# Kernel tuning notes

Measured on AMD Instinct MI355X. Metric: run time of the kernel, lower is better.

## Reference

```python
import jax, jax.numpy as jnp
import numpy as np

DIM = 1024
DIM_HEAD = 64
HEADS = 16
NUM_LATENTS = 64
INNER = DIM_HEAD * HEADS  # 1024


def setup_inputs() -> dict:
    key = jax.random.key(0)
    ks = jax.random.split(key, 6)
    b, m, n = 8, 4, 1024
    x = jax.random.normal(ks[0], (b, m, n, DIM), dtype=jnp.float32)
    latents = jax.random.normal(ks[1], (NUM_LATENTS, DIM), dtype=jnp.float32)
    # Linear weights stored as (in, out); no bias for q/kv, bias for out (matches nn.Linear defaults)
    Wq = jax.random.normal(ks[2], (DIM, INNER), dtype=jnp.float32) * (DIM ** -0.5)
    Wkv = jax.random.normal(ks[3], (DIM, INNER * 2), dtype=jnp.float32) * (DIM ** -0.5)
    Wout = jax.random.normal(ks[4], (INNER, DIM), dtype=jnp.float32) * (INNER ** -0.5)
    bout = jax.random.normal(ks[5], (DIM,), dtype=jnp.float32) * 0.01
    return {"x": x, "latents": latents, "Wq": Wq, "Wkv": Wkv, "Wout": Wout, "bout": bout}


def reference(x, latents, Wq, Wkv, Wout, bout):
    b, m, n, d = x.shape
    h, dh = HEADS, DIM_HEAD
    scale = dh ** -0.5

    # q from latents: [n_lat, inner] -> [h, i, dh]
    q = (latents @ Wq).reshape(NUM_LATENTS, h, dh).transpose(1, 0, 2) * scale

    # k, v from media tokens: [b, m, n, 2*inner] -> two [b, h, m, n, dh]
    kv = x @ Wkv
    k, v = jnp.split(kv, 2, axis=-1)
    k = k.reshape(b, m, n, h, dh).transpose(0, 3, 1, 2, 4)  # b h m n dh
    v = v.reshape(b, m, n, h, dh).transpose(0, 3, 1, 2, 4)

    # latent k, v: [n_lat, 2*inner] -> [h, n_lat, dh] broadcast to [b, h, m, n_lat, dh]
    lkv = latents @ Wkv
    lk, lv = jnp.split(lkv, 2, axis=-1)
    lk = jnp.broadcast_to(lk.reshape(NUM_LATENTS, h, dh).transpose(1, 0, 2)[None, :, None], (b, h, m, NUM_LATENTS, dh))
    lv = jnp.broadcast_to(lv.reshape(NUM_LATENTS, h, dh).transpose(1, 0, 2)[None, :, None], (b, h, m, NUM_LATENTS, dh))

    k = jnp.concatenate((k, lk), axis=-2)  # b h m (n + n_lat) dh
    v = jnp.concatenate((v, lv), axis=-2)

    sim = jnp.einsum('hid,bhmjd->bhmij', q, k)
    attn = jax.nn.softmax(sim, axis=-1)  # stable softmax (max-subtract internal)
    out = jnp.einsum('bhmij,bhmjd->bhmid', attn, v)  # b h m i dh
    out = out.transpose(0, 2, 3, 1, 4).reshape(b, m, NUM_LATENTS, h * dh)  # b m i inner
    return out @ Wout + bout
```

## Files before the change

kernel.cpp:

```cpp
#include <hip/hip_runtime.h>
#include <cstdint>

typedef __attribute__((ext_vector_type(8))) __bf16 bf16x8;
typedef __attribute__((ext_vector_type(4))) float f32x4;
typedef __attribute__((ext_vector_type(8))) unsigned short u16x8;
typedef __attribute__((ext_vector_type(4))) unsigned short u16x4;

__device__ __forceinline__ unsigned short f2bf(float f) {
    union { float f; unsigned u; } v; v.f = f;
    unsigned u = v.u;
    return (unsigned short)((u + 0x7FFFu + ((u >> 16) & 1u)) >> 16);
}

__device__ __forceinline__ void gload_lds16(const void* g, void* l) {
    auto gp = reinterpret_cast<__attribute__((address_space(1))) unsigned*>(
        reinterpret_cast<uintptr_t>(g));
    auto lp = reinterpret_cast<__attribute__((address_space(3))) unsigned*>(
        reinterpret_cast<uintptr_t>(l));
    __builtin_amdgcn_global_load_lds(gp, lp, 16, 0, 0);
}

__global__ __launch_bounds__(256) void cvt_kernel(const float* __restrict__ in,
                                                  unsigned short* __restrict__ out, int n4) {
    int idx = blockIdx.x * 256 + threadIdx.x;
    int stride = gridDim.x * 256;
    for (int i = idx; i < n4; i += stride) {
        float4 v = ((const float4*)in)[i];
        u16x4 o;
        o.x = f2bf(v.x); o.y = f2bf(v.y); o.z = f2bf(v.z); o.w = f2bf(v.w);
        ((u16x4*)out)[i] = o;
    }
}

__global__ __launch_bounds__(256) void transpose_cvt(const float* __restrict__ in,
                                                     unsigned short* __restrict__ out,
                                                     int R, int C) {
    __shared__ float t[32][33];
    int c0 = blockIdx.x * 32, r0 = blockIdx.y * 32;
    int tx = threadIdx.x, ty = threadIdx.y;
    for (int i = ty; i < 32; i += 8)
        t[i][tx] = in[(size_t)(r0 + i) * C + c0 + tx];
    __syncthreads();
    for (int i = ty; i < 32; i += 8)
        out[(size_t)(c0 + i) * R + r0 + tx] = f2bf(t[tx][i]);
}

__global__ __launch_bounds__(256) void gemm128p(const unsigned short* __restrict__ A,
                                                const unsigned short* __restrict__ Bt,
                                                void* __restrict__ C,
                                                const float* __restrict__ bias,
                                                int M, int N, int K, float scale, int split,
                                                int c_f32) {
    __shared__ unsigned short lds[3][2][4096];
    int ntx = N >> 7;
    int nwg = gridDim.x, bid = blockIdx.x, swz = bid;
    if ((nwg & 7) == 0) { int cpx = nwg >> 3; swz = (bid & 7) * cpx + (bid >> 3); }
    int m0 = (swz / ntx) << 7, n0 = (swz % ntx) << 7;
    int tid = threadIdx.x, lane = tid & 63, w = tid >> 6;
    int wm = w >> 1, wn = w & 1;
    int lr = lane & 15, lg = lane >> 4;
    int gq = lg ^ ((lr >> 1) & 3);
    int nkt = K >> 5;

    int arow = tid >> 2;
    int sgl = (tid & 3) ^ ((arow >> 1) & 3);
    int ra0 = m0 + arow;      if (ra0 > M - 1) ra0 = M - 1;
    int ra1 = m0 + 64 + arow; if (ra1 > M - 1) ra1 = M - 1;
    const unsigned short* a0 = A + (size_t)ra0 * K + (sgl << 3);
    const unsigned short* a1 = A + (size_t)ra1 * K + (sgl << 3);
    const unsigned short* b0 = Bt + (size_t)(n0 + arow) * K + (sgl << 3);
    const unsigned short* b1 = Bt + (size_t)(n0 + 64 + arow) * K + (sgl << 3);

    f32x4 acc[4][4] = {};

#define ST_A128(bi, kt) do { \
        gload_lds16(a0 + ((kt) << 5), &lds[bi][0][w << 9]); \
        gload_lds16(a1 + ((kt) << 5), &lds[bi][0][2048 + (w << 9)]); } while (0)
#define ST_B128(bi, kt) do { \
        gload_lds16(b0 + ((kt) << 5), &lds[bi][1][w << 9]); \
        gload_lds16(b1 + ((kt) << 5), &lds[bi][1][2048 + (w << 9)]); } while (0)

    ST_A128(0, 0); ST_B128(0, 0);
    ST_A128(1, 1); ST_B128(1, 1);

    int buf = 0;
    for (int t = 0; t < nkt; ++t) {
        asm volatile("s_waitcnt vmcnt(4) lgkmcnt(0)" ::: "memory");
        __builtin_amdgcn_sched_barrier(0);
        __builtin_amdgcn_s_barrier();
        __builtin_amdgcn_sched_barrier(0);
        int st = t + 2; if (st >= nkt) st = nkt - 1;
        int sbuf = buf + 2; if (sbuf >= 3) sbuf -= 3;
        ST_A128(sbuf, st);
        ST_B128(sbuf, st);
        const unsigned short* pa = &lds[buf][0][((wm << 6) + lr) * 32 + (gq << 3)];
        const unsigned short* pb = &lds[buf][1][((wn << 6) + lr) * 32 + (gq << 3)];
        bf16x8 af[4], bfr[4];
#pragma unroll
        for (int nt = 0; nt < 4; nt++) bfr[nt] = *(const bf16x8*)(pb + nt * 512);
#pragma unroll
        for (int mt = 0; mt < 4; mt++) af[mt] = *(const bf16x8*)(pa + mt * 512);
        __builtin_amdgcn_s_setprio(1);
#pragma unroll
        for (int mt = 0; mt < 4; mt++)
#pragma unroll
            for (int nt = 0; nt < 4; nt++)
                acc[mt][nt] = __builtin_amdgcn_mfma_f32_16x16x32_bf16(af[mt], bfr[nt], acc[mt][nt], 0, 0, 0);
        __builtin_amdgcn_s_setprio(0);
        buf++; if (buf == 3) buf = 0;
    }
#undef ST_A128
#undef ST_B128

#pragma unroll
    for (int mt = 0; mt < 4; mt++) {
#pragma unroll
        for (int nt = 0; nt < 4; nt++) {
            int col = n0 + (wn << 6) + (nt << 4) + lr;
            float sc = (col < split) ? scale : 1.0f;
            float bv = bias ? bias[col] : 0.0f;
#pragma unroll
            for (int r = 0; r < 4; r++) {
                int row = m0 + (wm << 6) + (mt << 4) + (lg << 2) + r;
                if (row < M) {
                    float v = acc[mt][nt][r] * sc + bv;
                    if (c_f32) ((float*)C)[(size_t)row * N + col] = v;
                    else       ((unsigned short*)C)[(size_t)row * N + col] = f2bf(v);
                }
            }
        }
    }
}

__global__ __launch_bounds__(512, 2) void gemm256(const unsigned short* __restrict__ A,
                                                  const unsigned short* __restrict__ Bt,
                                                  unsigned short* __restrict__ C,
                                                  int M, int N, int K) {
    __shared__ unsigned short lds[2][32768];
    int nkt = K >> 6;
    int ntx = N >> 8;
    int nwg = gridDim.x, bid = blockIdx.x, swz = bid;
    if ((nwg & 7) == 0) { int cpx = nwg >> 3; swz = (bid & 7) * cpx + (bid >> 3); }
    int m0 = (swz / ntx) << 8, n0 = (swz % ntx) << 8;
    int tid = threadIdx.x, lane = tid & 63, w = tid >> 6;
    int wm = w >> 2, wn = w & 3;
    int lr = lane & 15, lg = lane >> 4;

    int srow = lane >> 3;
    int sg = (lane & 7) ^ srow;
    const unsigned short* aS = A + (size_t)(m0 + (w << 3) + srow) * K + (sg << 3);
    const unsigned short* bS = Bt + (size_t)(n0 + (w << 3) + srow) * K + (sg << 3);
    size_t rs64 = (size_t)64 * K;

    int baseA = (wm << 13) + lr * 64;
    int baseB = 16384 + (wn << 12) + lr * 64;
    int kg0 = (((0 << 2) + lg) ^ (lr & 7)) << 3;
    int kg1 = (((1 << 2) + lg) ^ (lr & 7)) << 3;

    f32x4 acc[8][4] = {};

#define ST_A(bi, kt) do { \
        gload_lds16(aS + ((size_t)(kt) << 6),          &lds[bi][(w << 9)]); \
        gload_lds16(aS + rs64 + ((size_t)(kt) << 6),   &lds[bi][4096 + (w << 9)]); \
        gload_lds16(aS + 2*rs64 + ((size_t)(kt) << 6), &lds[bi][8192 + (w << 9)]); \
        gload_lds16(aS + 3*rs64 + ((size_t)(kt) << 6), &lds[bi][12288 + (w << 9)]); } while (0)
#define ST_B(bi, kt) do { \
        gload_lds16(bS + ((size_t)(kt) << 6),          &lds[bi][16384 + (w << 9)]); \
        gload_lds16(bS + rs64 + ((size_t)(kt) << 6),   &lds[bi][20480 + (w << 9)]); \
        gload_lds16(bS + 2*rs64 + ((size_t)(kt) << 6), &lds[bi][24576 + (w << 9)]); \
        gload_lds16(bS + 3*rs64 + ((size_t)(kt) << 6), &lds[bi][28672 + (w << 9)]); } while (0)

    ST_A(0, 0);
    ST_B(0, 0);

    for (int t = 0; t < nkt; ++t) {
        int cur = t & 1, nxt = cur ^ 1;
        int st = t + 1; if (st >= nkt) st = nkt - 1;
        const unsigned short* L = &lds[cur][0];
        bf16x8 af[4], bfr[4];

        ST_A(nxt, st);
        __builtin_amdgcn_sched_barrier(0);
        asm volatile("s_waitcnt vmcnt(4)" ::: "memory");
        __builtin_amdgcn_sched_barrier(0);
        __builtin_amdgcn_s_barrier();
        __builtin_amdgcn_sched_barrier(0);
#pragma unroll
        for (int nt = 0; nt < 4; nt++) bfr[nt] = *(const bf16x8*)(L + baseB + nt * 1024 + kg0);
#pragma unroll
        for (int i = 0; i < 4; i++) af[i] = *(const bf16x8*)(L + baseA + i * 1024 + kg0);
        asm volatile("s_waitcnt lgkmcnt(0)" ::: "memory");
        __builtin_amdgcn_sched_barrier(0);
        __builtin_amdgcn_s_setprio(1);
#pragma unroll
        for (int i = 0; i < 4; i++)
#pragma unroll
            for (int nt = 0; nt < 4; nt++)
                acc[i][nt] = __builtin_amdgcn_mfma_f32_16x16x32_bf16(af[i], bfr[nt], acc[i][nt], 0, 0, 0);
        __builtin_amdgcn_s_setprio(0);

        ST_B(nxt, st);
#pragma unroll
        for (int i = 0; i < 4; i++) af[i] = *(const bf16x8*)(L + baseA + (i + 4) * 1024 + kg0);
        asm volatile("s_waitcnt lgkmcnt(0)" ::: "memory");
        __builtin_amdgcn_sched_barrier(0);
        __builtin_amdgcn_s_setprio(1);
#pragma unroll
        for (int i = 0; i < 4; i++)
#pragma unroll
            for (int nt = 0; nt < 4; nt++)
                acc[i + 4][nt] = __builtin_amdgcn_mfma_f32_16x16x32_bf16(af[i], bfr[nt], acc[i + 4][nt], 0, 0, 0);
        __builtin_amdgcn_s_setprio(0);

#pragma unroll
        for (int nt = 0; nt < 4; nt++) bfr[nt] = *(const bf16x8*)(L + baseB + nt * 1024 + kg1);
#pragma unroll
        for (int i = 0; i < 4; i++) af[i] = *(const bf16x8*)(L + baseA + i * 1024 + kg1);
        asm volatile("s_waitcnt lgkmcnt(0)" ::: "memory");
        __builtin_amdgcn_sched_barrier(0);
        __builtin_amdgcn_s_setprio(1);
#pragma unroll
        for (int i = 0; i < 4; i++)
#pragma unroll
            for (int nt = 0; nt < 4; nt++)
                acc[i][nt] = __builtin_amdgcn_mfma_f32_16x16x32_bf16(af[i], bfr[nt], acc[i][nt], 0, 0, 0);
        __builtin_amdgcn_s_setprio(0);

#pragma unroll
        for (int i = 0; i < 4; i++) af[i] = *(const bf16x8*)(L + baseA + (i + 4) * 1024 + kg1);
        asm volatile("s_waitcnt lgkmcnt(0)" ::: "memory");
        __builtin_amdgcn_sched_barrier(0);
        __builtin_amdgcn_s_barrier();
        __builtin_amdgcn_sched_barrier(0);
        __builtin_amdgcn_s_setprio(1);
#pragma unroll
        for (int i = 0; i < 4; i++)
#pragma unroll
            for (int nt = 0; nt < 4; nt++)
                acc[i + 4][nt] = __builtin_amdgcn_mfma_f32_16x16x32_bf16(af[i], bfr[nt], acc[i + 4][nt], 0, 0, 0);
        __builtin_amdgcn_s_setprio(0);
    }
#undef ST_A
#undef ST_B

#pragma unroll
    for (int mt = 0; mt < 8; mt++) {
#pragma unroll
        for (int nt = 0; nt < 4; nt++) {
            int col = n0 + (wn << 6) + (nt << 4) + lr;
            size_t rbase = (size_t)(m0 + (wm << 7) + (mt << 4) + (lg << 2));
#pragma unroll
            for (int r = 0; r < 4; r++)
                C[(rbase + r) * N + col] = f2bf(acc[mt][nt][r]);
        }
    }
}

__global__ __launch_bounds__(256) void attn_kernel(const unsigned short* __restrict__ qg, int qstride,
                                                   const unsigned short* __restrict__ kvg,
                                                   const unsigned short* __restrict__ lkvg, int lstride,
                                                   unsigned short* __restrict__ og) {
    __shared__ unsigned short K_lds[64 * 72];
    __shared__ unsigned short V_lds[64 * 72];
    __shared__ unsigned short P_lds[4][16 * 72];
    int bm = blockIdx.x >> 4, h = blockIdx.x & 15;
    int tid = threadIdx.x, lane = tid & 63, w = tid >> 6;
    int lr = lane & 15, lg = lane >> 4;

    bf16x8 qf[2];
#pragma unroll
    for (int kk = 0; kk < 2; kk++)
        qf[kk] = *(const bf16x8*)(qg + (size_t)((w << 4) + lr) * qstride + (h << 6) + (kk << 5) + (lg << 3));

    f32x4 acc[4] = {};
    float m_run[4], l_run[4];
#pragma unroll
    for (int r = 0; r < 4; r++) { m_run[r] = -1e30f; l_run[r] = 0.0f; }

    int jrow = tid >> 2;
    int seg = (tid & 3) << 4;

    const unsigned short* s0 = kvg + (size_t)((bm << 10) + jrow) * 2048 + (h << 6);
    u16x8 k0 = *(const u16x8*)(s0 + seg);
    u16x8 k1 = *(const u16x8*)(s0 + seg + 8);
    u16x8 v0 = *(const u16x8*)(s0 + 1024 + seg);
    u16x8 v1 = *(const u16x8*)(s0 + 1024 + seg + 8);

    for (int t = 0; t < 17; t++) {
        *(u16x8*)(&K_lds[jrow * 72 + seg]) = k0;
        *(u16x8*)(&K_lds[jrow * 72 + seg + 8]) = k1;
#pragma unroll
        for (int c = 0; c < 8; c++) V_lds[(seg + c) * 72 + jrow] = v0[c];
#pragma unroll
        for (int c = 0; c < 8; c++) V_lds[(seg + 8 + c) * 72 + jrow] = v1[c];
        __syncthreads();

        u16x8 nk0 = k0, nk1 = k1, nv0 = v0, nv1 = v1;
        if (t < 16) {
            const unsigned short* src = (t < 15)
                ? kvg + (size_t)((bm << 10) + ((t + 1) << 6) + jrow) * 2048 + (h << 6)
                : lkvg + (size_t)jrow * lstride + (h << 6);
            nk0 = *(const u16x8*)(src + seg);
            nk1 = *(const u16x8*)(src + seg + 8);
            nv0 = *(const u16x8*)(src + 1024 + seg);
            nv1 = *(const u16x8*)(src + 1024 + seg + 8);
        }

        f32x4 s[4] = {};
#pragma unroll
        for (int jt = 0; jt < 4; jt++) {
#pragma unroll
            for (int kk = 0; kk < 2; kk++) {
                bf16x8 kf = *(const bf16x8*)(&K_lds[(size_t)((jt << 4) + lr) * 72 + (kk << 5) + (lg << 3)]);
                s[jt] = __builtin_amdgcn_mfma_f32_16x16x32_bf16(qf[kk], kf, s[jt], 0, 0, 0);
            }
        }
#pragma unroll
        for (int r = 0; r < 4; r++) {
            float mx = fmaxf(fmaxf(s[0][r], s[1][r]), fmaxf(s[2][r], s[3][r]));
            mx = fmaxf(mx, __shfl_xor(mx, 1));
            mx = fmaxf(mx, __shfl_xor(mx, 2));
            mx = fmaxf(mx, __shfl_xor(mx, 4));
            mx = fmaxf(mx, __shfl_xor(mx, 8));
            float nm = fmaxf(m_run[r], mx);
            float fct = __expf(m_run[r] - nm);
            m_run[r] = nm;
            float p0 = __expf(s[0][r] - nm);
            float p1 = __expf(s[1][r] - nm);
            float p2 = __expf(s[2][r] - nm);
            float p3 = __expf(s[3][r] - nm);
            float sum = p0 + p1 + p2 + p3;
            sum += __shfl_xor(sum, 1);
            sum += __shfl_xor(sum, 2);
            sum += __shfl_xor(sum, 4);
            sum += __shfl_xor(sum, 8);
            l_run[r] = l_run[r] * fct + sum;
#pragma unroll
            for (int dt = 0; dt < 4; dt++) acc[dt][r] *= fct;
            int prow = ((lg << 2) + r) * 72;
            P_lds[w][prow + lr]      = f2bf(p0);
            P_lds[w][prow + 16 + lr] = f2bf(p1);
            P_lds[w][prow + 32 + lr] = f2bf(p2);
            P_lds[w][prow + 48 + lr] = f2bf(p3);
        }
#pragma unroll
        for (int jkk = 0; jkk < 2; jkk++) {
            bf16x8 pf = *(const bf16x8*)(&P_lds[w][(size_t)lr * 72 + (jkk << 5) + (lg << 3)]);
#pragma unroll
            for (int dt = 0; dt < 4; dt++) {
                bf16x8 vf = *(const bf16x8*)(&V_lds[(size_t)((dt << 4) + lr) * 72 + (jkk << 5) + (lg << 3)]);
                acc[dt] = __builtin_amdgcn_mfma_f32_16x16x32_bf16(pf, vf, acc[dt], 0, 0, 0);
            }
        }
        __syncthreads();
        k0 = nk0; k1 = nk1; v0 = nv0; v1 = nv1;
    }
#pragma unroll
    for (int dt = 0; dt < 4; dt++) {
#pragma unroll
        for (int r = 0; r < 4; r++) {
            int i = (w << 4) + (lg << 2) + r;
            float v = acc[dt][r] / l_run[r];
            og[(size_t)((bm << 6) + i) * 1024 + (h << 6) + (dt << 4) + lr] = f2bf(v);
        }
    }
}

extern "C" void kernel_launch(void* const* d_in, const int* in_sizes, int n_in,
                              void* d_out, int out_size, void* d_ws, size_t ws_size,
                              hipStream_t stream) {
    const float* x       = (const float*)d_in[0];
    const float* latents = (const float*)d_in[1];
    const float* Wq      = (const float*)d_in[2];
    const float* Wkv     = (const float*)d_in[3];
    const float* Wout    = (const float*)d_in[4];
    const float* bout    = (const float*)d_in[5];
    char* ws = (char*)d_ws;
    unsigned short* xb    = (unsigned short*)(ws);
    unsigned short* kvb   = (unsigned short*)(ws + 67108864);
    unsigned short* wqkvt = (unsigned short*)(ws + 201326592);
    unsigned short* wkvt  = wqkvt + 1024 * 1024;
    unsigned short* woutt = (unsigned short*)(ws + 207618048);
    unsigned short* latb  = (unsigned short*)(ws + 209715200);
    unsigned short* qlkvb = (unsigned short*)(ws + 209846272);
    unsigned short* attnb = (unsigned short*)(ws + 210239488);

    cvt_kernel<<<2048, 256, 0, stream>>>(x, xb, 33554432 / 4);
    cvt_kernel<<<64, 256, 0, stream>>>(latents, latb, 65536 / 4);
    dim3 tb(32, 8);
    transpose_cvt<<<dim3(32, 32), tb, 0, stream>>>(Wq, wqkvt, 1024, 1024);
    transpose_cvt<<<dim3(64, 32), tb, 0, stream>>>(Wkv, wkvt, 1024, 2048);
    transpose_cvt<<<dim3(32, 32), tb, 0, stream>>>(Wout, woutt, 1024, 1024);
    gemm128p<<<24, 256, 0, stream>>>(latb, wqkvt, qlkvb, nullptr, 64, 3072, 1024, 0.125f, 1024, 0);
    gemm256<<<1024, 512, 0, stream>>>(xb, wkvt, kvb, 32768, 2048, 1024);
    attn_kernel<<<512, 256, 0, stream>>>(qlkvb, 3072, kvb, qlkvb + 1024, 3072, attnb);
    gemm128p<<<128, 256, 0, stream>>>(attnb, woutt, (void*)d_out, bout, 2048, 1024, 1024, 1.0f, 0, 1);
}
```

Measured before the change: 261.0 us.

## Store V transposed from projection GEMMs to avoid LDS scatter in attention

The KV projection GEMM now writes K and V to separate buffers, with V stored transposed per (batch·media, head-dim) row, and the latent projection GEMM writes latent V transposed too. The attention kernel can then load V tiles with vectorized row stores into LDS instead of 16 scalar transposed scatter stores per thread per tile. The cost is a less coalesced 4-element strided store pattern in the GEMM epilogue for V.

```diff
diff --git a/kernel.cpp b/kernel.cpp
--- a/kernel.cpp
+++ b/kernel.cpp
@@ -49,8 +49,9 @@
                                                 const unsigned short* __restrict__ Bt,
                                                 void* __restrict__ C,
                                                 const float* __restrict__ bias,
+                                                unsigned short* __restrict__ vT,
                                                 int M, int N, int K, float scale, int split,
-                                                int c_f32) {
+                                                int c_f32, int vstart) {
     __shared__ unsigned short lds[3][2][4096];
     int ntx = N >> 7;
     int nwg = gridDim.x, bid = blockIdx.x, swz = bid;
@@ -124,8 +125,9 @@
                 int row = m0 + (wm << 6) + (mt << 4) + (lg << 2) + r;
                 if (row < M) {
                     float v = acc[mt][nt][r] * sc + bv;
-                    if (c_f32) ((float*)C)[(size_t)row * N + col] = v;
-                    else       ((unsigned short*)C)[(size_t)row * N + col] = f2bf(v);
+                    if (vT && col >= vstart) vT[(size_t)(col - vstart) * 64 + row] = f2bf(v);
+                    else if (c_f32) ((float*)C)[(size_t)row * N + col] = v;
+                    else ((unsigned short*)C)[(size_t)row * N + col] = f2bf(v);
                 }
             }
         }
@@ -134,7 +136,8 @@
 
 __global__ __launch_bounds__(512, 2) void gemm256(const unsigned short* __restrict__ A,
                                                   const unsigned short* __restrict__ Bt,
-                                                  unsigned short* __restrict__ C,
+                                                  unsigned short* __restrict__ kb,
+                                                  unsigned short* __restrict__ vbT,
                                                   int M, int N, int K) {
     __shared__ unsigned short lds[2][32768];
     int nkt = K >> 6;
@@ -243,22 +246,40 @@
 #undef ST_A
 #undef ST_B
 
-#pragma unroll
-    for (int mt = 0; mt < 8; mt++) {
-#pragma unroll
-        for (int nt = 0; nt < 4; nt++) {
-            int col = n0 + (wn << 6) + (nt << 4) + lr;
-            size_t rbase = (size_t)(m0 + (wm << 7) + (mt << 4) + (lg << 2));
-#pragma unroll
-            for (int r = 0; r < 4; r++)
-                C[(rbase + r) * N + col] = f2bf(acc[mt][nt][r]);
+    if (n0 < 1024) {
+#pragma unroll
+        for (int mt = 0; mt < 8; mt++) {
+#pragma unroll
+            for (int nt = 0; nt < 4; nt++) {
+                int col = n0 + (wn << 6) + (nt << 4) + lr;
+                size_t rbase = (size_t)(m0 + (wm << 7) + (mt << 4) + (lg << 2));
+#pragma unroll
+                for (int r = 0; r < 4; r++)
+                    kb[(rbase + r) * 1024 + col] = f2bf(acc[mt][nt][r]);
+            }
+        }
+    } else {
+#pragma unroll
+        for (int mt = 0; mt < 8; mt++) {
+#pragma unroll
+            for (int nt = 0; nt < 4; nt++) {
+                int dg = n0 - 1024 + (wn << 6) + (nt << 4) + lr;
+                int rbase = m0 + (wm << 7) + (mt << 4) + (lg << 2);
+                int bm = rbase >> 10, j = rbase & 1023;
+                u16x4 o;
+                o.x = f2bf(acc[mt][nt][0]); o.y = f2bf(acc[mt][nt][1]);
+                o.z = f2bf(acc[mt][nt][2]); o.w = f2bf(acc[mt][nt][3]);
+                *(u16x4*)(&vbT[((size_t)(bm << 10) + dg) * 1024 + j]) = o;
+            }
         }
     }
 }
 
 __global__ __launch_bounds__(256) void attn_kernel(const unsigned short* __restrict__ qg, int qstride,
-                                                   const unsigned short* __restrict__ kvg,
-                                                   const unsigned short* __restrict__ lkvg, int lstride,
+                                                   const unsigned short* __restrict__ kb,
+                                                   const unsigned short* __restrict__ vbT,
+                                                   const unsigned short* __restrict__ lkg, int lstride,
+                                                   const unsigned short* __restrict__ lvT,
                                                    unsigned short* __restrict__ og) {
     __shared__ unsigned short K_lds[64 * 72];
     __shared__ unsigned short V_lds[64 * 72];
@@ -280,30 +301,37 @@
     int jrow = tid >> 2;
     int seg = (tid & 3) << 4;
 
-    const unsigned short* s0 = kvg + (size_t)((bm << 10) + jrow) * 2048 + (h << 6);
-    u16x8 k0 = *(const u16x8*)(s0 + seg);
-    u16x8 k1 = *(const u16x8*)(s0 + seg + 8);
-    u16x8 v0 = *(const u16x8*)(s0 + 1024 + seg);
-    u16x8 v1 = *(const u16x8*)(s0 + 1024 + seg + 8);
+    const unsigned short* k_s = kb + (size_t)((bm << 10) + jrow) * 1024 + (h << 6) + seg;
+    const unsigned short* v_s = vbT + (size_t)((bm << 10) + (h << 6) + jrow) * 1024 + seg;
+    u16x8 k0 = *(const u16x8*)(k_s);
+    u16x8 k1 = *(const u16x8*)(k_s + 8);
+    u16x8 v0 = *(const u16x8*)(v_s);
+    u16x8 v1 = *(const u16x8*)(v_s + 8);
 
     for (int t = 0; t < 17; t++) {
         *(u16x8*)(&K_lds[jrow * 72 + seg]) = k0;
         *(u16x8*)(&K_lds[jrow * 72 + seg + 8]) = k1;
-#pragma unroll
-        for (int c = 0; c < 8; c++) V_lds[(seg + c) * 72 + jrow] = v0[c];
-#pragma unroll
-        for (int c = 0; c < 8; c++) V_lds[(seg + 8 + c) * 72 + jrow] = v1[c];
+        *(u16x8*)(&V_lds[jrow * 72 + seg]) = v0;
+        *(u16x8*)(&V_lds[jrow * 72 + seg + 8]) = v1;
         __syncthreads();
 
         u16x8 nk0 = k0, nk1 = k1, nv0 = v0, nv1 = v1;
         if (t < 16) {
-            const unsigned short* src = (t < 15)
-                ? kvg + (size_t)((bm << 10) + ((t + 1) << 6) + jrow) * 2048 + (h << 6)
-                : lkvg + (size_t)jrow * lstride + (h << 6);
-            nk0 = *(const u16x8*)(src + seg);
-            nk1 = *(const u16x8*)(src + seg + 8);
-            nv0 = *(const u16x8*)(src + 1024 + seg);
-            nv1 = *(const u16x8*)(src + 1024 + seg + 8);
+            if (t < 15) {
+                const unsigned short* ks = kb + (size_t)((bm << 10) + ((t + 1) << 6) + jrow) * 1024 + (h << 6) + seg;
+                const unsigned short* vs = vbT + (size_t)((bm << 10) + (h << 6) + jrow) * 1024 + ((t + 1) << 6) + seg;
+                nk0 = *(const u16x8*)(ks);
+                nk1 = *(const u16x8*)(ks + 8);
+                nv0 = *(const u16x8*)(vs);
+                nv1 = *(const u16x8*)(vs + 8);
+            } else {
+                const unsigned short* ks = lkg + (size_t)jrow * lstride + (h << 6) + seg;
+                const unsigned short* vs = lvT + (size_t)((h << 6) + jrow) * 64 + seg;
+                nk0 = *(const u16x8*)(ks);
+                nk1 = *(const u16x8*)(ks + 8);
+                nv0 = *(const u16x8*)(vs);
+                nv1 = *(const u16x8*)(vs + 8);
+            }
         }
 
         f32x4 s[4] = {};
@@ -377,13 +405,15 @@
     const float* bout    = (const float*)d_in[5];
     char* ws = (char*)d_ws;
     unsigned short* xb    = (unsigned short*)(ws);
-    unsigned short* kvb   = (unsigned short*)(ws + 67108864);
+    unsigned short* kb    = (unsigned short*)(ws + 67108864);
+    unsigned short* vbT   = (unsigned short*)(ws + 134217728);
     unsigned short* wqkvt = (unsigned short*)(ws + 201326592);
     unsigned short* wkvt  = wqkvt + 1024 * 1024;
     unsigned short* woutt = (unsigned short*)(ws + 207618048);
     unsigned short* latb  = (unsigned short*)(ws + 209715200);
     unsigned short* qlkvb = (unsigned short*)(ws + 209846272);
     unsigned short* attnb = (unsigned short*)(ws + 210239488);
+    unsigned short* lvT   = (unsigned short*)(ws + 214433792);
 
     cvt_kernel<<<2048, 256, 0, stream>>>(x, xb, 33554432 / 4);
     cvt_kernel<<<64, 256, 0, stream>>>(latents, latb, 65536 / 4);
@@ -391,8 +421,8 @@
     transpose_cvt<<<dim3(32, 32), tb, 0, stream>>>(Wq, wqkvt, 1024, 1024);
     transpose_cvt<<<dim3(64, 32), tb, 0, stream>>>(Wkv, wkvt, 1024, 2048);
     transpose_cvt<<<dim3(32, 32), tb, 0, stream>>>(Wout, woutt, 1024, 1024);
-    gemm128p<<<24, 256, 0, stream>>>(latb, wqkvt, qlkvb, nullptr, 64, 3072, 1024, 0.125f, 1024, 0);
-    gemm256<<<1024, 512, 0, stream>>>(xb, wkvt, kvb, 32768, 2048, 1024);
-    attn_kernel<<<512, 256, 0, stream>>>(qlkvb, 3072, kvb, qlkvb + 1024, 3072, attnb);
-    gemm128p<<<128, 256, 0, stream>>>(attnb, woutt, (void*)d_out, bout, 2048, 1024, 1024, 1.0f, 0, 1);
-}
+    gemm128p<<<24, 256, 0, stream>>>(latb, wqkvt, qlkvb, nullptr, lvT, 64, 3072, 1024, 0.125f, 1024, 0, 2048);
+    gemm256<<<1024, 512, 0, stream>>>(xb, wkvt, kb, vbT, 32768, 2048, 1024);
+    attn_kernel<<<512, 256, 0, stream>>>(qlkvb, 3072, kb, vbT, qlkvb + 1024, 3072, lvT, attnb);
+    gemm128p<<<128, 256, 0, stream>>>(attnb, woutt, (void*)d_out, bout, nullptr, 2048, 1024, 1024, 1.0f, 0, 1, 1 << 30);
+}
```

Result: no change. 257.7 us (-1.3%).
